# Performance work log

Measured on AMD Instinct MI355X. Metric: run time of the kernel, lower is better.

Reference implementation:

```python
import jax, jax.numpy as jnp
import numpy as np

N_CELLS = 100000
IN_CH = 64
N_EDGES = 1280000


def setup_inputs() -> dict:
    key = jax.random.key(0)
    k1, k2, k3, k4, k5 = jax.random.split(key, 5)
    x_source = jax.random.normal(k1, (N_CELLS, IN_CH), dtype=jnp.float32)
    att_weight = jax.random.normal(k2, (2 * IN_CH,), dtype=jnp.float32)
    nbhd_values = jax.random.uniform(k3, (N_EDGES,), dtype=jnp.float32)
    target_index_i = jnp.sort(jax.random.randint(k4, (N_EDGES,), 0, N_CELLS))
    source_index_j = jax.random.randint(k5, (N_EDGES,), 0, N_CELLS)
    return {
        "x_source": x_source,
        "att_weight": att_weight,
        "nbhd_values": nbhd_values,
        "target_index_i": target_index_i,
        "source_index_j": source_index_j,
    }


def reference(x_source, att_weight, nbhd_values, target_index_i, source_index_j):
    # gather per-message endpoint features: [E, C] each
    x_src_msg = x_source[source_index_j]
    x_tgt_msg = x_source[target_index_i]  # x_target is None -> use x_source
    # attention: elu(cat([src, tgt]) @ w) -> [E]
    att = jax.nn.elu(
        jnp.concatenate([x_src_msg, x_tgt_msg], axis=1) @ att_weight
    )
    # modulate sparse neighborhood values by attention, scale messages
    vals = nbhd_values * att  # [E]
    x_message = vals[:, None] * x_src_msg  # [E, C]
    # scatter-sum into target cells: [N, C]
    return jax.ops.segment_sum(x_message, target_index_i, num_segments=N_CELLS)
```

## Files before the change

kernel.cpp:

```cpp
#include <hip/hip_runtime.h>

#define N_CELLS 100000
#define IN_CH 64
#define N_EDGES 1280000

__device__ __forceinline__ unsigned short f32_to_bf16(float f) {
    unsigned u = __float_as_uint(f);
    u += 0x7FFFu + ((u >> 16) & 1u);
    return (unsigned short)(u >> 16);
}
__device__ __forceinline__ float bf16_to_f32(unsigned short h) {
    return __uint_as_float((unsigned)h << 16);
}

#define SCORE_BLOCKS ((N_CELLS * 16 + 255) / 256)
#define ROWSTART_BLOCKS ((N_EDGES + 255) / 256)

__global__ void __launch_bounds__(256) prep_kernel(
    const float* __restrict__ x, const float* __restrict__ w,
    const int* __restrict__ tgt,
    float* __restrict__ s_src, float* __restrict__ s_tgt,
    unsigned short* __restrict__ xb, int* __restrict__ row_start,
    int n_cells, int n_edges) {
    if (blockIdx.x < SCORE_BLOCKS) {
        int gid  = blockIdx.x * 256 + threadIdx.x;
        int wave = gid >> 6;
        int lane = threadIdx.x & 63;
        int grp  = lane >> 4;
        int sub  = lane & 15;
        int cell = wave * 4 + grp;

        float4 xv = make_float4(0.f, 0.f, 0.f, 0.f);
        if (cell < n_cells)
            xv = *(const float4*)&x[(((unsigned)cell << 6) | ((unsigned)sub << 2))];
        if (xb && cell < n_cells) {
            ushort4 hb;
            hb.x = f32_to_bf16(xv.x); hb.y = f32_to_bf16(xv.y);
            hb.z = f32_to_bf16(xv.z); hb.w = f32_to_bf16(xv.w);
            *(ushort4*)&xb[(((unsigned)cell << 6) | ((unsigned)sub << 2))] = hb;
        }
        const float4* w4 = (const float4*)w;
        float4 wa = w4[sub];
        float4 wb = w4[16 + sub];
        float a = xv.x * wa.x + xv.y * wa.y + xv.z * wa.z + xv.w * wa.w;
        float b = xv.x * wb.x + xv.y * wb.y + xv.z * wb.z + xv.w * wb.w;
#pragma unroll
        for (int off = 8; off; off >>= 1) {
            a += __shfl_xor(a, off, 64);
            b += __shfl_xor(b, off, 64);
        }
        if (sub == 0 && cell < n_cells) {
            s_src[cell] = a;
            s_tgt[cell] = b;
        }
    } else {
        int e = (blockIdx.x - SCORE_BLOCKS) * 256 + threadIdx.x;
        if (e >= n_edges) return;
        int lane = threadIdx.x & 63;
        int t = tgt[e];
        int prev = __shfl_up(t, 1, 64);
        if (lane == 0) prev = (e == 0) ? -1 : tgt[e - 1];
        for (int c = prev + 1; c <= t; ++c) row_start[c] = e;
        if (e == n_edges - 1) {
            for (int c = t + 1; c <= n_cells; ++c) row_start[c] = n_edges;
        }
    }
}

__global__ void __launch_bounds__(256) agg_kernel_bf16(
    const unsigned short* __restrict__ xb, const int* __restrict__ src,
    const float* __restrict__ nbhd,
    const float* __restrict__ s_src, const float* __restrict__ s_tgt,
    const int* __restrict__ row_start,
    float* __restrict__ out, int n_cells) {
    int gid  = blockIdx.x * blockDim.x + threadIdx.x;
    int lane = threadIdx.x & 63;
    int grp  = lane >> 4;
    int sub  = lane & 15;
    int cell = (gid >> 6) * 4 + grp;
    unsigned suboff = (unsigned)sub << 2;
    int gbase = grp << 4;

    int lo = 0, hi = 0;
    float sti = 0.f;
    if (cell < n_cells) {
        lo  = row_start[cell];
        hi  = row_start[cell + 1];
        sti = s_tgt[cell];
    }

    float4 acc = make_float4(0.f, 0.f, 0.f, 0.f);
    for (int base = lo; base < hi; base += 16) {
        int cnt = hi - base;
        if (cnt > 16) cnt = 16;
        int   key = 0x7FFFFFFF;
        float v   = 0.f;
        if (sub < cnt) {
            int j = src[base + sub];
            float a = s_src[j] + sti;
            v = nbhd[base + sub] * (a > 0.f ? a : expm1f(a));
            key = j;
        }
#pragma unroll
        for (int size = 2; size <= 16; size <<= 1) {
#pragma unroll
            for (int strd = size >> 1; strd > 0; strd >>= 1) {
                int   pk = __shfl_xor(key, strd, 64);
                float pv = __shfl_xor(v,   strd, 64);
                bool takeMin = ((sub & size) == 0) == ((sub & strd) == 0);
                bool sw = takeMin ? (pk < key) : (pk > key);
                if (sw) { key = pk; v = pv; }
            }
        }
        int j = key;
        int t = 0;
        for (; t + 4 <= cnt; t += 4) {
            int   j0 = __shfl(j, gbase + t,     64);
            int   j1 = __shfl(j, gbase + t + 1, 64);
            int   j2 = __shfl(j, gbase + t + 2, 64);
            int   j3 = __shfl(j, gbase + t + 3, 64);
            float v0 = __shfl(v, gbase + t,     64);
            float v1 = __shfl(v, gbase + t + 1, 64);
            float v2 = __shfl(v, gbase + t + 2, 64);
            float v3 = __shfl(v, gbase + t + 3, 64);
            ushort4 h0 = *(const ushort4*)&xb[(((unsigned)j0 << 6) | suboff)];
            ushort4 h1 = *(const ushort4*)&xb[(((unsigned)j1 << 6) | suboff)];
            ushort4 h2 = *(const ushort4*)&xb[(((unsigned)j2 << 6) | suboff)];
            ushort4 h3 = *(const ushort4*)&xb[(((unsigned)j3 << 6) | suboff)];
            acc.x = fmaf(v0, bf16_to_f32(h0.x), acc.x);
            acc.y = fmaf(v0, bf16_to_f32(h0.y), acc.y);
            acc.z = fmaf(v0, bf16_to_f32(h0.z), acc.z);
            acc.w = fmaf(v0, bf16_to_f32(h0.w), acc.w);
            acc.x = fmaf(v1, bf16_to_f32(h1.x), acc.x);
            acc.y = fmaf(v1, bf16_to_f32(h1.y), acc.y);
            acc.z = fmaf(v1, bf16_to_f32(h1.z), acc.z);
            acc.w = fmaf(v1, bf16_to_f32(h1.w), acc.w);
            acc.x = fmaf(v2, bf16_to_f32(h2.x), acc.x);
            acc.y = fmaf(v2, bf16_to_f32(h2.y), acc.y);
            acc.z = fmaf(v2, bf16_to_f32(h2.z), acc.z);
            acc.w = fmaf(v2, bf16_to_f32(h2.w), acc.w);
            acc.x = fmaf(v3, bf16_to_f32(h3.x), acc.x);
            acc.y = fmaf(v3, bf16_to_f32(h3.y), acc.y);
            acc.z = fmaf(v3, bf16_to_f32(h3.z), acc.z);
            acc.w = fmaf(v3, bf16_to_f32(h3.w), acc.w);
        }
        for (; t < cnt; ++t) {
            int   jt = __shfl(j, gbase + t, 64);
            float vt = __shfl(v, gbase + t, 64);
            ushort4 ht = *(const ushort4*)&xb[(((unsigned)jt << 6) | suboff)];
            acc.x = fmaf(vt, bf16_to_f32(ht.x), acc.x);
            acc.y = fmaf(vt, bf16_to_f32(ht.y), acc.y);
            acc.z = fmaf(vt, bf16_to_f32(ht.z), acc.z);
            acc.w = fmaf(vt, bf16_to_f32(ht.w), acc.w);
        }
    }
    if (cell < n_cells)
        *(float4*)&out[(((unsigned)cell << 6) | suboff)] = acc;
}

__global__ void __launch_bounds__(256) agg_kernel_f32(
    const float* __restrict__ x, const int* __restrict__ src,
    const float* __restrict__ nbhd,
    const float* __restrict__ s_src, const float* __restrict__ s_tgt,
    const int* __restrict__ row_start,
    float* __restrict__ out, int n_cells) {
    int gid  = blockIdx.x * blockDim.x + threadIdx.x;
    int lane = threadIdx.x & 63;
    int grp  = lane >> 4;
    int sub  = lane & 15;
    int cell = (gid >> 6) * 4 + grp;
    unsigned suboff = (unsigned)sub << 2;
    int gbase = grp << 4;

    int lo = 0, hi = 0;
    float sti = 0.f;
    if (cell < n_cells) {
        lo  = row_start[cell];
        hi  = row_start[cell + 1];
        sti = s_tgt[cell];
    }
    float4 acc = make_float4(0.f, 0.f, 0.f, 0.f);
    for (int base = lo; base < hi; base += 16) {
        int cnt = hi - base;
        if (cnt > 16) cnt = 16;
        int   j = 0;
        float v = 0.f;
        if (sub < cnt) {
            j = src[base + sub];
            float a = s_src[j] + sti;
            v = nbhd[base + sub] * (a > 0.f ? a : expm1f(a));
        }
        for (int t = 0; t < cnt; ++t) {
            int   jt = __shfl(j, gbase + t, 64);
            float vt = __shfl(v, gbase + t, 64);
            float4 xt = *(const float4*)&x[(((unsigned)jt << 6) | suboff)];
            acc.x = fmaf(vt, xt.x, acc.x); acc.y = fmaf(vt, xt.y, acc.y);
            acc.z = fmaf(vt, xt.z, acc.z); acc.w = fmaf(vt, xt.w, acc.w);
        }
    }
    if (cell < n_cells)
        *(float4*)&out[(((unsigned)cell << 6) | suboff)] = acc;
}

extern "C" void kernel_launch(void* const* d_in, const int* in_sizes, int n_in,
                              void* d_out, int out_size, void* d_ws, size_t ws_size,
                              hipStream_t stream) {
    const float* x    = (const float*)d_in[0];
    const float* w    = (const float*)d_in[1];
    const float* nbhd = (const float*)d_in[2];
    const int*   tgt  = (const int*)d_in[3];
    const int*   src  = (const int*)d_in[4];
    float*       out  = (float*)d_out;

    float* s_src     = (float*)d_ws;
    float* s_tgt     = s_src + N_CELLS;
    int*   row_start = (int*)(s_tgt + N_CELLS);
    unsigned short* xb = (unsigned short*)(row_start + N_CELLS + 1);
    size_t need_bf16 = (size_t)(2 * N_CELLS + N_CELLS + 1) * 4 + (size_t)N_CELLS * IN_CH * 2;
    bool use_bf16 = ws_size >= need_bf16;

    {
        int blocks = SCORE_BLOCKS + ROWSTART_BLOCKS;
        prep_kernel<<<blocks, 256, 0, stream>>>(x, w, tgt, s_src, s_tgt,
                                                use_bf16 ? xb : (unsigned short*)nullptr,
                                                row_start, N_CELLS, N_EDGES);
    }
    {
        int threads = 256;
        int blocks  = (N_CELLS * 16 + threads - 1) / threads;
        if (use_bf16)
            agg_kernel_bf16<<<blocks, threads, 0, stream>>>(xb, src, nbhd, s_src, s_tgt,
                                                            row_start, out, N_CELLS);
        else
            agg_kernel_f32<<<blocks, threads, 0, stream>>>(x, src, nbhd, s_src, s_tgt,
                                                           row_start, out, N_CELLS);
    }
}
```

Before: 62.08 us.

## Split bf16 features into channel halves and drop per-chunk bitonic sort

```diff
diff --git a/kernel.cpp b/kernel.cpp
--- a/kernel.cpp
+++ b/kernel.cpp
@@ -9,8 +9,11 @@
     u += 0x7FFFu + ((u >> 16) & 1u);
     return (unsigned short)(u >> 16);
 }
-__device__ __forceinline__ float bf16_to_f32(unsigned short h) {
-    return __uint_as_float((unsigned)h << 16);
+__device__ __forceinline__ float bf16_lo(unsigned h) {
+    return __uint_as_float(h << 16);
+}
+__device__ __forceinline__ float bf16_hi(unsigned h) {
+    return __uint_as_float(h & 0xFFFF0000u);
 }
 
 #define SCORE_BLOCKS ((N_CELLS * 16 + 255) / 256)
@@ -37,7 +40,9 @@
             ushort4 hb;
             hb.x = f32_to_bf16(xv.x); hb.y = f32_to_bf16(xv.y);
             hb.z = f32_to_bf16(xv.z); hb.w = f32_to_bf16(xv.w);
-            *(ushort4*)&xb[(((unsigned)cell << 6) | ((unsigned)sub << 2))] = hb;
+            unsigned idx = (unsigned)(sub >> 3) * ((unsigned)n_cells << 5)
+                         + ((unsigned)cell << 5) + (((unsigned)sub & 7) << 2);
+            *(ushort4*)&xb[idx] = hb;
         }
         const float4* w4 = (const float4*)w;
         float4 wa = w4[sub];
@@ -67,7 +72,7 @@
     }
 }
 
-__global__ void __launch_bounds__(256) agg_kernel_bf16(
+__global__ void __launch_bounds__(256) agg_kernel_split(
     const unsigned short* __restrict__ xb, const int* __restrict__ src,
     const float* __restrict__ nbhd,
     const float* __restrict__ s_src, const float* __restrict__ s_tgt,
@@ -77,42 +82,29 @@
     int lane = threadIdx.x & 63;
     int grp  = lane >> 4;
     int sub  = lane & 15;
-    int cell = (gid >> 6) * 4 + grp;
-    unsigned suboff = (unsigned)sub << 2;
+    int g    = (gid >> 6) * 4 + grp;
+    int half = (g >= n_cells) ? 1 : 0;
+    int cell = g - half * n_cells;
+    if (cell >= n_cells) return;
     int gbase = grp << 4;
-
-    int lo = 0, hi = 0;
-    float sti = 0.f;
-    if (cell < n_cells) {
-        lo  = row_start[cell];
-        hi  = row_start[cell + 1];
-        sti = s_tgt[cell];
-    }
-
-    float4 acc = make_float4(0.f, 0.f, 0.f, 0.f);
+    const unsigned short* xh = xb + (size_t)half * ((size_t)n_cells << 5);
+    unsigned choff = (unsigned)sub << 1;
+
+    int lo  = row_start[cell];
+    int hi  = row_start[cell + 1];
+    float sti = s_tgt[cell];
+
+    float2 acc = make_float2(0.f, 0.f);
     for (int base = lo; base < hi; base += 16) {
         int cnt = hi - base;
         if (cnt > 16) cnt = 16;
-        int   key = 0x7FFFFFFF;
-        float v   = 0.f;
+        int   j = 0;
+        float v = 0.f;
         if (sub < cnt) {
-            int j = src[base + sub];
+            j = src[base + sub];
             float a = s_src[j] + sti;
             v = nbhd[base + sub] * (a > 0.f ? a : expm1f(a));
-            key = j;
-        }
-#pragma unroll
-        for (int size = 2; size <= 16; size <<= 1) {
-#pragma unroll
-            for (int strd = size >> 1; strd > 0; strd >>= 1) {
-                int   pk = __shfl_xor(key, strd, 64);
-                float pv = __shfl_xor(v,   strd, 64);
-                bool takeMin = ((sub & size) == 0) == ((sub & strd) == 0);
-                bool sw = takeMin ? (pk < key) : (pk > key);
-                if (sw) { key = pk; v = pv; }
-            }
-        }
-        int j = key;
+        }
         int t = 0;
         for (; t + 4 <= cnt; t += 4) {
             int   j0 = __shfl(j, gbase + t,     64);
@@ -123,39 +115,28 @@
             float v1 = __shfl(v, gbase + t + 1, 64);
             float v2 = __shfl(v, gbase + t + 2, 64);
             float v3 = __shfl(v, gbase + t + 3, 64);
-            ushort4 h0 = *(const ushort4*)&xb[(((unsigned)j0 << 6) | suboff)];
-            ushort4 h1 = *(const ushort4*)&xb[(((unsigned)j1 << 6) | suboff)];
-            ushort4 h2 = *(const ushort4*)&xb[(((unsigned)j2 << 6) | suboff)];
-            ushort4 h3 = *(const ushort4*)&xb[(((unsigned)j3 << 6) | suboff)];
-            acc.x = fmaf(v0, bf16_to_f32(h0.x), acc.x);
-            acc.y = fmaf(v0, bf16_to_f32(h0.y), acc.y);
-            acc.z = fmaf(v0, bf16_to_f32(h0.z), acc.z);
-            acc.w = fmaf(v0, bf16_to_f32(h0.w), acc.w);
-            acc.x = fmaf(v1, bf16_to_f32(h1.x), acc.x);
-            acc.y = fmaf(v1, bf16_to_f32(h1.y), acc.y);
-            acc.z = fmaf(v1, bf16_to_f32(h1.z), acc.z);
-            acc.w = fmaf(v1, bf16_to_f32(h1.w), acc.w);
-            acc.x = fmaf(v2, bf16_to_f32(h2.x), acc.x);
-            acc.y = fmaf(v2, bf16_to_f32(h2.y), acc.y);
-            acc.z = fmaf(v2, bf16_to_f32(h2.z), acc.z);
-            acc.w = fmaf(v2, bf16_to_f32(h2.w), acc.w);
-            acc.x = fmaf(v3, bf16_to_f32(h3.x), acc.x);
-            acc.y = fmaf(v3, bf16_to_f32(h3.y), acc.y);
-            acc.z = fmaf(v3, bf16_to_f32(h3.z), acc.z);
-            acc.w = fmaf(v3, bf16_to_f32(h3.w), acc.w);
+            unsigned h0 = *(const unsigned*)&xh[(((unsigned)j0 << 5) | choff)];
+            unsigned h1 = *(const unsigned*)&xh[(((unsigned)j1 << 5) | choff)];
+            unsigned h2 = *(const unsigned*)&xh[(((unsigned)j2 << 5) | choff)];
+            unsigned h3 = *(const unsigned*)&xh[(((unsigned)j3 << 5) | choff)];
+            acc.x = fmaf(v0, bf16_lo(h0), acc.x);
+            acc.y = fmaf(v0, bf16_hi(h0), acc.y);
+            acc.x = fmaf(v1, bf16_lo(h1), acc.x);
+            acc.y = fmaf(v1, bf16_hi(h1), acc.y);
+            acc.x = fmaf(v2, bf16_lo(h2), acc.x);
+            acc.y = fmaf(v2, bf16_hi(h2), acc.y);
+            acc.x = fmaf(v3, bf16_lo(h3), acc.x);
+            acc.y = fmaf(v3, bf16_hi(h3), acc.y);
         }
         for (; t < cnt; ++t) {
             int   jt = __shfl(j, gbase + t, 64);
             float vt = __shfl(v, gbase + t, 64);
-            ushort4 ht = *(const ushort4*)&xb[(((unsigned)jt << 6) | suboff)];
-            acc.x = fmaf(vt, bf16_to_f32(ht.x), acc.x);
-            acc.y = fmaf(vt, bf16_to_f32(ht.y), acc.y);
-            acc.z = fmaf(vt, bf16_to_f32(ht.z), acc.z);
-            acc.w = fmaf(vt, bf16_to_f32(ht.w), acc.w);
-        }
-    }
-    if (cell < n_cells)
-        *(float4*)&out[(((unsigned)cell << 6) | suboff)] = acc;
+            unsigned ht = *(const unsigned*)&xh[(((unsigned)jt << 5) | choff)];
+            acc.x = fmaf(vt, bf16_lo(ht), acc.x);
+            acc.y = fmaf(vt, bf16_hi(ht), acc.y);
+        }
+    }
+    *(float2*)&out[(((unsigned)cell << 6) | ((unsigned)half << 5) | choff)] = acc;
 }
 
 __global__ void __launch_bounds__(256) agg_kernel_f32(
@@ -225,14 +206,15 @@
                                                 use_bf16 ? xb : (unsigned short*)nullptr,
                                                 row_start, N_CELLS, N_EDGES);
     }
-    {
+    if (use_bf16) {
+        int threads = 256;
+        int blocks  = (2 * N_CELLS * 16 + threads - 1) / threads;
+        agg_kernel_split<<<blocks, threads, 0, stream>>>(xb, src, nbhd, s_src, s_tgt,
+                                                         row_start, out, N_CELLS);
+    } else {
         int threads = 256;
         int blocks  = (N_CELLS * 16 + threads - 1) / threads;
-        if (use_bf16)
-            agg_kernel_bf16<<<blocks, threads, 0, stream>>>(xb, src, nbhd, s_src, s_tgt,
-                                                            row_start, out, N_CELLS);
-        else
-            agg_kernel_f32<<<blocks, threads, 0, stream>>>(x, src, nbhd, s_src, s_tgt,
-                                                           row_start, out, N_CELLS);
-    }
-}
+        agg_kernel_f32<<<blocks, threads, 0, stream>>>(x, src, nbhd, s_src, s_tgt,
+                                                       row_start, out, N_CELLS);
+    }
+}
```

New measurement: 68.36 us. 1.1x slower.
